# Kernel optimization log

Measured on AMD Instinct MI355X. Metric: run time of the kernel, lower is better.

The kernel has to match this reference:

```python
import jax, jax.numpy as jnp
import numpy as np

NUM_NODES = 50000
NUM_EDGES = 600000
HIDDEN = 128


def setup_inputs() -> dict:
    key = jax.random.key(0)
    ks = jax.random.split(key, 8)
    edge_index = jax.random.randint(ks[0], (2, NUM_EDGES), 0, NUM_NODES, dtype=jnp.int32)
    # xavier-uniform-ish init for node embeddings and GCN weights
    lim_emb = float(np.sqrt(6.0 / (NUM_NODES + HIDDEN)))
    node_emb = jax.random.uniform(ks[1], (NUM_NODES, HIDDEN), jnp.float32, -lim_emb, lim_emb)
    lim_w = float(np.sqrt(6.0 / (HIDDEN + HIDDEN)))
    W0 = jax.random.uniform(ks[2], (HIDDEN, HIDDEN), jnp.float32, -lim_w, lim_w)
    W1 = jax.random.uniform(ks[3], (HIDDEN, HIDDEN), jnp.float32, -lim_w, lim_w)
    W2 = jax.random.uniform(ks[4], (HIDDEN, HIDDEN), jnp.float32, -lim_w, lim_w)
    b0 = jnp.zeros((HIDDEN,), jnp.float32)
    b1 = jnp.zeros((HIDDEN,), jnp.float32)
    b2 = jnp.zeros((HIDDEN,), jnp.float32)
    return {"edge_index": edge_index, "node_emb": node_emb,
            "W0": W0, "b0": b0, "W1": W1, "b1": b1, "W2": W2, "b2": b2}


def _gcn_conv(x, W, b, src, dst, norm, n):
    # PyG GCNConv: linear transform, then sym-normalized scatter-sum + bias
    h = x @ W                                  # [N, H]
    msg = h[src] * norm[:, None]               # [E+N, H] gather + scale
    out = jax.ops.segment_sum(msg, dst, num_segments=n)  # scatter-sum
    return out + b


def reference(edge_index, node_emb, W0, b0, W1, b1, W2, b2):
    n = node_emb.shape[0]
    loop = jnp.arange(n, dtype=edge_index.dtype)
    src = jnp.concatenate([edge_index[0], loop])   # add self-loops
    dst = jnp.concatenate([edge_index[1], loop])
    deg = jnp.zeros((n,), node_emb.dtype).at[dst].add(1.0)
    dinv = jax.lax.rsqrt(deg)                      # deg >= 1 due to self-loops
    norm = dinv[src] * dinv[dst]                   # [E+N]

    x = node_emb
    x = _gcn_conv(x, W0, b0, src, dst, norm, n)
    x = jax.nn.relu(x)                             # dropout in eval mode: identity
    x = _gcn_conv(x, W1, b1, src, dst, norm, n)
    x = jax.nn.relu(x)
    x = _gcn_conv(x, W2, b2, src, dst, norm, n)
    return x
```

## Files before the change

### kernel.cpp

```cpp
#include <hip/hip_runtime.h>
#include <hip/hip_fp16.h>

#define N_NODES 50000
#define N_EDGES 600000
#define HID 128
#define CAP 64

typedef _Float16 half8 __attribute__((ext_vector_type(8)));
typedef float f32x4 __attribute__((ext_vector_type(4)));

union Pack8 {
    _Float16 h[8];
    uint4 u;
};


__global__ __launch_bounds__(256) void k_init(int* __restrict__ cnt,
                                              const float* __restrict__ W0,
                                              const float* __restrict__ W1,
                                              const float* __restrict__ W2,
                                              _Float16* __restrict__ Wt) {
    int i = blockIdx.x * 256 + threadIdx.x;
    if (i < N_NODES) cnt[i] = 0;
    if (i < 3 * HID * HID) {
        int l = i >> 14;
        int r = i & 16383;
        int n = r >> 7, k = r & 127;
        const float* W = (l == 0) ? W0 : (l == 1) ? W1 : W2;
        Wt[i] = (_Float16)W[k * HID + n];
    }
}


__global__ __launch_bounds__(256) void k_bucket(const int* __restrict__ src,
                                                const int* __restrict__ dst,
                                                int* __restrict__ cnt,
                                                int* __restrict__ bkt) {
    int e = blockIdx.x * 256 + threadIdx.x;
    if (e >= N_EDGES) return;
    int d = dst[e];
    int pos = atomicAdd(&cnt[d], 1);
    if (pos < CAP) bkt[d * CAP + pos] = src[e];
}


__global__ __launch_bounds__(512) void k_gemm0(const float* __restrict__ X,
                                               const _Float16* __restrict__ Wt,
                                               const int* __restrict__ cnt,
                                               _Float16* __restrict__ HS) {
    __shared__ _Float16 Xl[128][136];
    __shared__ _Float16 Wl[128][136];

    const int tid = threadIdx.x;
    const int row0 = blockIdx.x * 128;

#pragma unroll
    for (int j = 0; j < 8; ++j) {
        int idx = tid + j * 512;
        int r = idx >> 5, p = idx & 31;
        float4 v = make_float4(0.f, 0.f, 0.f, 0.f);
        if (row0 + r < N_NODES) v = ((const float4*)X)[(size_t)(row0 + r) * 32 + p];
        _Float16* d = &Xl[r][p * 4];
        d[0] = (_Float16)v.x; d[1] = (_Float16)v.y;
        d[2] = (_Float16)v.z; d[3] = (_Float16)v.w;
    }
#pragma unroll
    for (int j = 0; j < 4; ++j) {
        int idx = tid + j * 512;
        int r = idx >> 4, p = idx & 15;
        *(uint4*)&Wl[r][p * 8] = ((const uint4*)Wt)[idx];
    }
    __syncthreads();

    const int w = tid >> 6;
    const int l = tid & 63;
    const int m16 = l & 15;
    const int kg = l >> 4;

    f32x4 acc[8];
#pragma unroll
    for (int nt = 0; nt < 8; ++nt) acc[nt] = (f32x4)(0.f);
#pragma unroll
    for (int ks = 0; ks < 4; ++ks) {
        half8 a = *(const half8*)&Xl[w * 16 + m16][kg * 8 + ks * 32];
#pragma unroll
        for (int nt = 0; nt < 8; ++nt) {
            half8 b = *(const half8*)&Wl[nt * 16 + m16][kg * 8 + ks * 32];
            acc[nt] = __builtin_amdgcn_mfma_f32_16x16x32_f16(a, b, acc[nt], 0, 0, 0);
        }
    }

    const int rbase = row0 + w * 16 + kg * 4;
#pragma unroll
    for (int j = 0; j < 4; ++j) {
        int r = rbase + j;
        if (r < N_NODES) {
            float dv = rsqrtf((float)(cnt[r] + 1));
#pragma unroll
            for (int nt = 0; nt < 8; ++nt)
                HS[(size_t)r * HID + nt * 16 + m16] = (_Float16)(acc[nt][j] * dv);
        }
    }
}


__global__ __launch_bounds__(512) void k_fused(const _Float16* __restrict__ hsIn,
                                               const int* __restrict__ bkt,
                                               const int* __restrict__ cnt,
                                               const float* __restrict__ bias,
                                               const _Float16* __restrict__ Wt,
                                               _Float16* __restrict__ hsOut) {
    __shared__ _Float16 Xl[128][136];
    __shared__ _Float16 Wl[128][136];

    const int tid = threadIdx.x;
    const int row0 = blockIdx.x * 128;

#pragma unroll
    for (int j = 0; j < 4; ++j) {
        int idx = tid + j * 512;
        int r = idx >> 4, p = idx & 15;
        *(uint4*)&Wl[r][p * 8] = ((const uint4*)Wt)[idx];
    }

    const int grp = tid >> 4;
    const int c = (tid & 15) * 8;
    const _Float16* __restrict__ hc = hsIn + c;
    float4 bv0 = *(const float4*)&bias[c];
    float4 bv1 = *(const float4*)&bias[c + 4];
    float bb[8] = {bv0.x, bv0.y, bv0.z, bv0.w, bv1.x, bv1.y, bv1.z, bv1.w};

#pragma unroll
    for (int rnd = 0; rnd < 4; ++rnd) {
        int rl = rnd * 32 + grp;
        int node = row0 + rl;
        Pack8 pk;
        if (node < N_NODES) {
            float a[8], a2[8];
            {
                Pack8 v;
                v.u = *(const uint4*)&hc[(size_t)node * HID];
#pragma unroll
                for (int j = 0; j < 8; ++j) { a[j] = (float)v.h[j]; a2[j] = 0.f; }
            }
            const int* __restrict__ row = bkt + node * CAP;
            int ne = cnt[node];
            int e = 0;
            for (; e + 4 <= ne; e += 4) {
                int4 s4 = *(const int4*)&row[e];
                Pack8 v0, v1, v2, v3;
                v0.u = *(const uint4*)&hc[(size_t)s4.x * HID];
                v1.u = *(const uint4*)&hc[(size_t)s4.y * HID];
                v2.u = *(const uint4*)&hc[(size_t)s4.z * HID];
                v3.u = *(const uint4*)&hc[(size_t)s4.w * HID];
#pragma unroll
                for (int j = 0; j < 8; ++j) {
                    a[j] += (float)v0.h[j] + (float)v1.h[j];
                    a2[j] += (float)v2.h[j] + (float)v3.h[j];
                }
            }
            if (e + 2 <= ne) {
                int s0 = row[e], s1 = row[e + 1];
                Pack8 v0, v1;
                v0.u = *(const uint4*)&hc[(size_t)s0 * HID];
                v1.u = *(const uint4*)&hc[(size_t)s1 * HID];
#pragma unroll
                for (int j = 0; j < 8; ++j) a[j] += (float)v0.h[j] + (float)v1.h[j];
                e += 2;
            }
            if (e < ne) {
                int s0 = row[e];
                Pack8 v0;
                v0.u = *(const uint4*)&hc[(size_t)s0 * HID];
#pragma unroll
                for (int j = 0; j < 8; ++j) a[j] += (float)v0.h[j];
            }
            float dv = rsqrtf((float)(ne + 1));
#pragma unroll
            for (int j = 0; j < 8; ++j)
                pk.h[j] = (_Float16)fmaxf(bb[j] + dv * (a[j] + a2[j]), 0.f);
        } else {
            pk.u = make_uint4(0, 0, 0, 0);
        }
        *(uint4*)&Xl[rl][c] = pk.u;
    }
    __syncthreads();

    const int w = tid >> 6;
    const int l = tid & 63;
    const int m16 = l & 15;
    const int kg = l >> 4;

    f32x4 acc[8];
#pragma unroll
    for (int nt = 0; nt < 8; ++nt) acc[nt] = (f32x4)(0.f);
#pragma unroll
    for (int ks = 0; ks < 4; ++ks) {
        half8 a = *(const half8*)&Xl[w * 16 + m16][kg * 8 + ks * 32];
#pragma unroll
        for (int nt = 0; nt < 8; ++nt) {
            half8 b = *(const half8*)&Wl[nt * 16 + m16][kg * 8 + ks * 32];
            acc[nt] = __builtin_amdgcn_mfma_f32_16x16x32_f16(a, b, acc[nt], 0, 0, 0);
        }
    }

    const int rbase = row0 + w * 16 + kg * 4;
#pragma unroll
    for (int j = 0; j < 4; ++j) {
        int r = rbase + j;
        if (r < N_NODES) {
            float dv = rsqrtf((float)(cnt[r] + 1));
#pragma unroll
            for (int nt = 0; nt < 8; ++nt)
                hsOut[(size_t)r * HID + nt * 16 + m16] = (_Float16)(acc[nt][j] * dv);
        }
    }
}


__global__ __launch_bounds__(256) void k_gather_out(const _Float16* __restrict__ hs,
                                                    const int* __restrict__ bkt,
                                                    const int* __restrict__ cnt,
                                                    const float* __restrict__ bias,
                                                    float* __restrict__ out) {
    int t = blockIdx.x * 256 + threadIdx.x;
    int node = t >> 4;
    if (node >= N_NODES) return;
    int c = (t & 15) * 8;

    const _Float16* __restrict__ hc = hs + c;

    float a[8], a2[8];
    {
        Pack8 v;
        v.u = *(const uint4*)&hc[(size_t)node * HID];
#pragma unroll
        for (int j = 0; j < 8; ++j) { a[j] = (float)v.h[j]; a2[j] = 0.f; }
    }
    const int* __restrict__ row = bkt + node * CAP;
    int ne = cnt[node];
    int e = 0;
    for (; e + 4 <= ne; e += 4) {
        int4 s4 = *(const int4*)&row[e];
        Pack8 v0, v1, v2, v3;
        v0.u = *(const uint4*)&hc[(size_t)s4.x * HID];
        v1.u = *(const uint4*)&hc[(size_t)s4.y * HID];
        v2.u = *(const uint4*)&hc[(size_t)s4.z * HID];
        v3.u = *(const uint4*)&hc[(size_t)s4.w * HID];
#pragma unroll
        for (int j = 0; j < 8; ++j) {
            a[j] += (float)v0.h[j] + (float)v1.h[j];
            a2[j] += (float)v2.h[j] + (float)v3.h[j];
        }
    }
    if (e + 2 <= ne) {
        int s0 = row[e], s1 = row[e + 1];
        Pack8 v0, v1;
        v0.u = *(const uint4*)&hc[(size_t)s0 * HID];
        v1.u = *(const uint4*)&hc[(size_t)s1 * HID];
#pragma unroll
        for (int j = 0; j < 8; ++j) a[j] += (float)v0.h[j] + (float)v1.h[j];
        e += 2;
    }
    if (e < ne) {
        int s0 = row[e];
        Pack8 v0;
        v0.u = *(const uint4*)&hc[(size_t)s0 * HID];
#pragma unroll
        for (int j = 0; j < 8; ++j) a[j] += (float)v0.h[j];
    }

    float dv = rsqrtf((float)(ne + 1));
    float4 b0 = *(const float4*)&bias[c];
    float4 b1 = *(const float4*)&bias[c + 4];
    float bb[8] = {b0.x, b0.y, b0.z, b0.w, b1.x, b1.y, b1.z, b1.w};
    float4* op = (float4*)&out[(size_t)node * HID + c];
    op[0] = make_float4(bb[0] + dv * (a[0] + a2[0]), bb[1] + dv * (a[1] + a2[1]),
                        bb[2] + dv * (a[2] + a2[2]), bb[3] + dv * (a[3] + a2[3]));
    op[1] = make_float4(bb[4] + dv * (a[4] + a2[4]), bb[5] + dv * (a[5] + a2[5]),
                        bb[6] + dv * (a[6] + a2[6]), bb[7] + dv * (a[7] + a2[7]));
}


extern "C" void kernel_launch(void* const* d_in, const int* in_sizes, int n_in,
                              void* d_out, int out_size, void* d_ws, size_t ws_size,
                              hipStream_t stream) {
    const int* edge_index = (const int*)d_in[0];
    const float* node_emb = (const float*)d_in[1];
    const float* W0 = (const float*)d_in[2];
    const float* b0 = (const float*)d_in[3];
    const float* W1 = (const float*)d_in[4];
    const float* b1 = (const float*)d_in[5];
    const float* W2 = (const float*)d_in[6];
    const float* b2 = (const float*)d_in[7];
    float* out = (float*)d_out;

    const int* src = edge_index;
    const int* dst = edge_index + N_EDGES;

    float* ws = (float*)d_ws;
    int* cnt = (int*)ws;
    int* bkt = (int*)(ws + 50000);
    _Float16* hsA = (_Float16*)(ws + 3250000);
    _Float16* hsB = (_Float16*)(ws + 6450000);
    _Float16* Wt = (_Float16*)(ws + 9650000);

    const int tile_blocks = (N_NODES + 127) / 128;
    const int gath_blocks = (N_NODES * 16 + 255) / 256;
    const int edge_blocks = (N_EDGES + 255) / 256;
    const int init_blocks = (N_NODES + 255) / 256;

    k_init<<<init_blocks, 256, 0, stream>>>(cnt, W0, W1, W2, Wt);
    k_bucket<<<edge_blocks, 256, 0, stream>>>(src, dst, cnt, bkt);

    k_gemm0<<<tile_blocks, 512, 0, stream>>>(node_emb, Wt, cnt, hsA);
    k_fused<<<tile_blocks, 512, 0, stream>>>(hsA, bkt, cnt, b0, Wt + 16384, hsB);
    k_fused<<<tile_blocks, 512, 0, stream>>>(hsB, bkt, cnt, b1, Wt + 32768, hsA);
    k_gather_out<<<gath_blocks, 256, 0, stream>>>(hsA, bkt, cnt, b2, out);
}
```

Baseline: 158.7 us.

## Sort tile rows by degree to balance gather work across wavefronts

Adds a per-tile counting sort of the 128 nodes by in-degree in shared memory and uses the permutation to assign nodes to 16-lane groups in the fused aggregation and final gather kernels. Nodes with similar degree then share a wavefront, which cuts lane divergence in the variable-length neighbor loops. The final gather kernel is restructured to 512-thread tile blocks handling 4 rounds of nodes each. The cost is extra syncthreads and shared-memory atomics per block, plus fewer, larger blocks in the output kernel.

```diff
diff --git a/kernel.cpp b/kernel.cpp
--- a/kernel.cpp
+++ b/kernel.cpp
@@ -104,6 +104,35 @@
 }
 
 
+__device__ __forceinline__ void tile_sort(int tid, int row0,
+                                          const int* __restrict__ cnt,
+                                          unsigned char* tperm, short* lne,
+                                          int* lhist, int* lcur) {
+    if (tid < 64) { lhist[tid] = 0; lcur[tid] = 0; }
+    __syncthreads();
+    int myne = 0;
+    if (tid < 128) {
+        int node = row0 + tid;
+        myne = (node < N_NODES) ? cnt[node] : 0;
+        lne[tid] = (short)myne;
+        atomicAdd(&lhist[myne < 63 ? myne : 63], 1);
+    }
+    __syncthreads();
+    if (tid == 0) {
+        int s = 0;
+#pragma unroll
+        for (int b = 0; b < 64; ++b) { int x = lhist[b]; lhist[b] = s; s += x; }
+    }
+    __syncthreads();
+    if (tid < 128) {
+        int b = myne < 63 ? myne : 63;
+        int pos = lhist[b] + atomicAdd(&lcur[b], 1);
+        tperm[pos] = (unsigned char)tid;
+    }
+    __syncthreads();
+}
+
+
 __global__ __launch_bounds__(512) void k_fused(const _Float16* __restrict__ hsIn,
                                                const int* __restrict__ bkt,
                                                const int* __restrict__ cnt,
@@ -112,6 +141,9 @@
                                                _Float16* __restrict__ hsOut) {
     __shared__ _Float16 Xl[128][136];
     __shared__ _Float16 Wl[128][136];
+    __shared__ int lhist[64], lcur[64];
+    __shared__ unsigned char tperm[128];
+    __shared__ short lne[128];
 
     const int tid = threadIdx.x;
     const int row0 = blockIdx.x * 128;
@@ -122,6 +154,8 @@
         int r = idx >> 4, p = idx & 15;
         *(uint4*)&Wl[r][p * 8] = ((const uint4*)Wt)[idx];
     }
+
+    tile_sort(tid, row0, cnt, tperm, lne, lhist, lcur);
 
     const int grp = tid >> 4;
     const int c = (tid & 15) * 8;
@@ -132,7 +166,7 @@
 
 #pragma unroll
     for (int rnd = 0; rnd < 4; ++rnd) {
-        int rl = rnd * 32 + grp;
+        int rl = tperm[rnd * 32 + grp];
         int node = row0 + rl;
         Pack8 pk;
         if (node < N_NODES) {
@@ -144,7 +178,7 @@
                 for (int j = 0; j < 8; ++j) { a[j] = (float)v.h[j]; a2[j] = 0.f; }
             }
             const int* __restrict__ row = bkt + node * CAP;
-            int ne = cnt[node];
+            int ne = lne[rl];
             int e = 0;
             for (; e + 4 <= ne; e += 4) {
                 int4 s4 = *(const int4*)&row[e];
@@ -218,67 +252,79 @@
 }
 
 
-__global__ __launch_bounds__(256) void k_gather_out(const _Float16* __restrict__ hs,
+__global__ __launch_bounds__(512) void k_gather_out(const _Float16* __restrict__ hs,
                                                     const int* __restrict__ bkt,
                                                     const int* __restrict__ cnt,
                                                     const float* __restrict__ bias,
                                                     float* __restrict__ out) {
-    int t = blockIdx.x * 256 + threadIdx.x;
-    int node = t >> 4;
-    if (node >= N_NODES) return;
-    int c = (t & 15) * 8;
-
+    __shared__ int lhist[64], lcur[64];
+    __shared__ unsigned char tperm[128];
+    __shared__ short lne[128];
+
+    const int tid = threadIdx.x;
+    const int row0 = blockIdx.x * 128;
+
+    tile_sort(tid, row0, cnt, tperm, lne, lhist, lcur);
+
+    const int grp = tid >> 4;
+    const int c = (tid & 15) * 8;
     const _Float16* __restrict__ hc = hs + c;
-
-    float a[8], a2[8];
-    {
-        Pack8 v;
-        v.u = *(const uint4*)&hc[(size_t)node * HID];
-#pragma unroll
-        for (int j = 0; j < 8; ++j) { a[j] = (float)v.h[j]; a2[j] = 0.f; }
-    }
-    const int* __restrict__ row = bkt + node * CAP;
-    int ne = cnt[node];
-    int e = 0;
-    for (; e + 4 <= ne; e += 4) {
-        int4 s4 = *(const int4*)&row[e];
-        Pack8 v0, v1, v2, v3;
-        v0.u = *(const uint4*)&hc[(size_t)s4.x * HID];
-        v1.u = *(const uint4*)&hc[(size_t)s4.y * HID];
-        v2.u = *(const uint4*)&hc[(size_t)s4.z * HID];
-        v3.u = *(const uint4*)&hc[(size_t)s4.w * HID];
-#pragma unroll
-        for (int j = 0; j < 8; ++j) {
-            a[j] += (float)v0.h[j] + (float)v1.h[j];
-            a2[j] += (float)v2.h[j] + (float)v3.h[j];
-        }
-    }
-    if (e + 2 <= ne) {
-        int s0 = row[e], s1 = row[e + 1];
-        Pack8 v0, v1;
-        v0.u = *(const uint4*)&hc[(size_t)s0 * HID];
-        v1.u = *(const uint4*)&hc[(size_t)s1 * HID];
-#pragma unroll
-        for (int j = 0; j < 8; ++j) a[j] += (float)v0.h[j] + (float)v1.h[j];
-        e += 2;
-    }
-    if (e < ne) {
-        int s0 = row[e];
-        Pack8 v0;
-        v0.u = *(const uint4*)&hc[(size_t)s0 * HID];
-#pragma unroll
-        for (int j = 0; j < 8; ++j) a[j] += (float)v0.h[j];
-    }
-
-    float dv = rsqrtf((float)(ne + 1));
-    float4 b0 = *(const float4*)&bias[c];
-    float4 b1 = *(const float4*)&bias[c + 4];
-    float bb[8] = {b0.x, b0.y, b0.z, b0.w, b1.x, b1.y, b1.z, b1.w};
-    float4* op = (float4*)&out[(size_t)node * HID + c];
-    op[0] = make_float4(bb[0] + dv * (a[0] + a2[0]), bb[1] + dv * (a[1] + a2[1]),
-                        bb[2] + dv * (a[2] + a2[2]), bb[3] + dv * (a[3] + a2[3]));
-    op[1] = make_float4(bb[4] + dv * (a[4] + a2[4]), bb[5] + dv * (a[5] + a2[5]),
-                        bb[6] + dv * (a[6] + a2[6]), bb[7] + dv * (a[7] + a2[7]));
+    float4 bv0 = *(const float4*)&bias[c];
+    float4 bv1 = *(const float4*)&bias[c + 4];
+    float bb[8] = {bv0.x, bv0.y, bv0.z, bv0.w, bv1.x, bv1.y, bv1.z, bv1.w};
+
+#pragma unroll
+    for (int rnd = 0; rnd < 4; ++rnd) {
+        int rl = tperm[rnd * 32 + grp];
+        int node = row0 + rl;
+        if (node >= N_NODES) continue;
+        float a[8], a2[8];
+        {
+            Pack8 v;
+            v.u = *(const uint4*)&hc[(size_t)node * HID];
+#pragma unroll
+            for (int j = 0; j < 8; ++j) { a[j] = (float)v.h[j]; a2[j] = 0.f; }
+        }
+        const int* __restrict__ row = bkt + node * CAP;
+        int ne = lne[rl];
+        int e = 0;
+        for (; e + 4 <= ne; e += 4) {
+            int4 s4 = *(const int4*)&row[e];
+            Pack8 v0, v1, v2, v3;
+            v0.u = *(const uint4*)&hc[(size_t)s4.x * HID];
+            v1.u = *(const uint4*)&hc[(size_t)s4.y * HID];
+            v2.u = *(const uint4*)&hc[(size_t)s4.z * HID];
+            v3.u = *(const uint4*)&hc[(size_t)s4.w * HID];
+#pragma unroll
+            for (int j = 0; j < 8; ++j) {
+                a[j] += (float)v0.h[j] + (float)v1.h[j];
+                a2[j] += (float)v2.h[j] + (float)v3.h[j];
+            }
+        }
+        if (e + 2 <= ne) {
+            int s0 = row[e], s1 = row[e + 1];
+            Pack8 v0, v1;
+            v0.u = *(const uint4*)&hc[(size_t)s0 * HID];
+            v1.u = *(const uint4*)&hc[(size_t)s1 * HID];
+#pragma unroll
+            for (int j = 0; j < 8; ++j) a[j] += (float)v0.h[j] + (float)v1.h[j];
+            e += 2;
+        }
+        if (e < ne) {
+            int s0 = row[e];
+            Pack8 v0;
+            v0.u = *(const uint4*)&hc[(size_t)s0 * HID];
+#pragma unroll
+            for (int j = 0; j < 8; ++j) a[j] += (float)v0.h[j];
+        }
+
+        float dv = rsqrtf((float)(ne + 1));
+        float4* op = (float4*)&out[(size_t)node * HID + c];
+        op[0] = make_float4(bb[0] + dv * (a[0] + a2[0]), bb[1] + dv * (a[1] + a2[1]),
+                            bb[2] + dv * (a[2] + a2[2]), bb[3] + dv * (a[3] + a2[3]));
+        op[1] = make_float4(bb[4] + dv * (a[4] + a2[4]), bb[5] + dv * (a[5] + a2[5]),
+                            bb[6] + dv * (a[6] + a2[6]), bb[7] + dv * (a[7] + a2[7]));
+    }
 }
 
 
@@ -306,7 +352,6 @@
     _Float16* Wt = (_Float16*)(ws + 9650000);
 
     const int tile_blocks = (N_NODES + 127) / 128;
-    const int gath_blocks = (N_NODES * 16 + 255) / 256;
     const int edge_blocks = (N_EDGES + 255) / 256;
     const int init_blocks = (N_NODES + 255) / 256;
 
@@ -316,5 +361,5 @@
     k_gemm0<<<tile_blocks, 512, 0, stream>>>(node_emb, Wt, cnt, hsA);
     k_fused<<<tile_blocks, 512, 0, stream>>>(hsA, bkt, cnt, b0, Wt + 16384, hsB);
     k_fused<<<tile_blocks, 512, 0, stream>>>(hsB, bkt, cnt, b1, Wt + 32768, hsA);
-    k_gather_out<<<gath_blocks, 256, 0, stream>>>(hsA, bkt, cnt, b2, out);
-}
+    k_gather_out<<<tile_blocks, 512, 0, stream>>>(hsA, bkt, cnt, b2, out);
+}
```

Result: no change. 158.3 us, median of 2 (-0.2%).

## Halve fused tile to 64 rows and sort rows by degree for gather balance

Applied to the files above, without the earlier changes.

The fused gather+GEMM kernel now processes 64 nodes per block instead of 128, doubling the block count, and raises the occupancy hint via launch bounds. Within each block, nodes are counting-sorted by in-degree so that 16-lane groups handling rows in the same round have similar edge counts, reducing divergence and tail imbalance. The GEMM stage is re-split so each of the eight waves computes a 16x64 quarter tile. The cost is extra shared-memory histogram work and syncs, plus reloading W into LDS for twice as many blocks.

```diff
diff --git a/kernel.cpp b/kernel.cpp
--- a/kernel.cpp
+++ b/kernel.cpp
@@ -104,17 +104,20 @@
 }
 
 
-__global__ __launch_bounds__(512) void k_fused(const _Float16* __restrict__ hsIn,
-                                               const int* __restrict__ bkt,
-                                               const int* __restrict__ cnt,
-                                               const float* __restrict__ bias,
-                                               const _Float16* __restrict__ Wt,
-                                               _Float16* __restrict__ hsOut) {
-    __shared__ _Float16 Xl[128][136];
+__global__ __launch_bounds__(512, 6) void k_fused(const _Float16* __restrict__ hsIn,
+                                                  const int* __restrict__ bkt,
+                                                  const int* __restrict__ cnt,
+                                                  const float* __restrict__ bias,
+                                                  const _Float16* __restrict__ Wt,
+                                                  _Float16* __restrict__ hsOut) {
+    __shared__ _Float16 Xl[64][136];
     __shared__ _Float16 Wl[128][136];
+    __shared__ int lhist[64], lcur[64];
+    __shared__ unsigned char tperm[64];
+    __shared__ short lne[64];
 
     const int tid = threadIdx.x;
-    const int row0 = blockIdx.x * 128;
+    const int row0 = blockIdx.x * 64;
 
 #pragma unroll
     for (int j = 0; j < 4; ++j) {
@@ -122,6 +125,29 @@
         int r = idx >> 4, p = idx & 15;
         *(uint4*)&Wl[r][p * 8] = ((const uint4*)Wt)[idx];
     }
+
+    if (tid < 64) { lhist[tid] = 0; lcur[tid] = 0; }
+    __syncthreads();
+    int myne = 0;
+    if (tid < 64) {
+        int node = row0 + tid;
+        myne = (node < N_NODES) ? cnt[node] : 0;
+        lne[tid] = (short)myne;
+        atomicAdd(&lhist[myne < 63 ? myne : 63], 1);
+    }
+    __syncthreads();
+    if (tid == 0) {
+        int s = 0;
+#pragma unroll
+        for (int b = 0; b < 64; ++b) { int x = lhist[b]; lhist[b] = s; s += x; }
+    }
+    __syncthreads();
+    if (tid < 64) {
+        int b = myne < 63 ? myne : 63;
+        int pos = lhist[b] + atomicAdd(&lcur[b], 1);
+        tperm[pos] = (unsigned char)tid;
+    }
+    __syncthreads();
 
     const int grp = tid >> 4;
     const int c = (tid & 15) * 8;
@@ -131,8 +157,8 @@
     float bb[8] = {bv0.x, bv0.y, bv0.z, bv0.w, bv1.x, bv1.y, bv1.z, bv1.w};
 
 #pragma unroll
-    for (int rnd = 0; rnd < 4; ++rnd) {
-        int rl = rnd * 32 + grp;
+    for (int rnd = 0; rnd < 2; ++rnd) {
+        int rl = tperm[rnd * 32 + grp];
         int node = row0 + rl;
         Pack8 pk;
         if (node < N_NODES) {
@@ -144,7 +170,7 @@
                 for (int j = 0; j < 8; ++j) { a[j] = (float)v.h[j]; a2[j] = 0.f; }
             }
             const int* __restrict__ row = bkt + node * CAP;
-            int ne = cnt[node];
+            int ne = lne[rl];
             int e = 0;
             for (; e + 4 <= ne; e += 4) {
                 int4 s4 = *(const int4*)&row[e];
@@ -187,32 +213,34 @@
     __syncthreads();
 
     const int w = tid >> 6;
+    const int wr = w >> 1;
+    const int wc = w & 1;
     const int l = tid & 63;
     const int m16 = l & 15;
     const int kg = l >> 4;
 
-    f32x4 acc[8];
-#pragma unroll
-    for (int nt = 0; nt < 8; ++nt) acc[nt] = (f32x4)(0.f);
+    f32x4 acc[4];
+#pragma unroll
+    for (int nt = 0; nt < 4; ++nt) acc[nt] = (f32x4)(0.f);
 #pragma unroll
     for (int ks = 0; ks < 4; ++ks) {
-        half8 a = *(const half8*)&Xl[w * 16 + m16][kg * 8 + ks * 32];
-#pragma unroll
-        for (int nt = 0; nt < 8; ++nt) {
-            half8 b = *(const half8*)&Wl[nt * 16 + m16][kg * 8 + ks * 32];
+        half8 a = *(const half8*)&Xl[wr * 16 + m16][kg * 8 + ks * 32];
+#pragma unroll
+        for (int nt = 0; nt < 4; ++nt) {
+            half8 b = *(const half8*)&Wl[wc * 64 + nt * 16 + m16][kg * 8 + ks * 32];
             acc[nt] = __builtin_amdgcn_mfma_f32_16x16x32_f16(a, b, acc[nt], 0, 0, 0);
         }
     }
 
-    const int rbase = row0 + w * 16 + kg * 4;
+    const int rbase = row0 + wr * 16 + kg * 4;
 #pragma unroll
     for (int j = 0; j < 4; ++j) {
         int r = rbase + j;
         if (r < N_NODES) {
             float dv = rsqrtf((float)(cnt[r] + 1));
 #pragma unroll
-            for (int nt = 0; nt < 8; ++nt)
-                hsOut[(size_t)r * HID + nt * 16 + m16] = (_Float16)(acc[nt][j] * dv);
+            for (int nt = 0; nt < 4; ++nt)
+                hsOut[(size_t)r * HID + wc * 64 + nt * 16 + m16] = (_Float16)(acc[nt][j] * dv);
         }
     }
 }
@@ -305,7 +333,8 @@
     _Float16* hsB = (_Float16*)(ws + 6450000);
     _Float16* Wt = (_Float16*)(ws + 9650000);
 
-    const int tile_blocks = (N_NODES + 127) / 128;
+    const int gemm_blocks = (N_NODES + 127) / 128;
+    const int fuse_blocks = (N_NODES + 63) / 64;
     const int gath_blocks = (N_NODES * 16 + 255) / 256;
     const int edge_blocks = (N_EDGES + 255) / 256;
     const int init_blocks = (N_NODES + 255) / 256;
@@ -313,8 +342,8 @@
     k_init<<<init_blocks, 256, 0, stream>>>(cnt, W0, W1, W2, Wt);
     k_bucket<<<edge_blocks, 256, 0, stream>>>(src, dst, cnt, bkt);
 
-    k_gemm0<<<tile_blocks, 512, 0, stream>>>(node_emb, Wt, cnt, hsA);
-    k_fused<<<tile_blocks, 512, 0, stream>>>(hsA, bkt, cnt, b0, Wt + 16384, hsB);
-    k_fused<<<tile_blocks, 512, 0, stream>>>(hsB, bkt, cnt, b1, Wt + 32768, hsA);
+    k_gemm0<<<gemm_blocks, 512, 0, stream>>>(node_emb, Wt, cnt, hsA);
+    k_fused<<<fuse_blocks, 512, 0, stream>>>(hsA, bkt, cnt, b0, Wt + 16384, hsB);
+    k_fused<<<fuse_blocks, 512, 0, stream>>>(hsB, bkt, cnt, b1, Wt + 32768, hsA);
     k_gather_out<<<gath_blocks, 256, 0, stream>>>(hsA, bkt, cnt, b2, out);
 }
```

After: 172.8 us. +8.9%, slower.

## Slice features into column panels, compact CSR with 16-bit indices, unfuse gather from GEMM

Applied to the files above, without the earlier changes.

Stores intermediate features in eight 16-column slices so each gather block works on one 32-byte slice per node, aiming to keep the gathered working set of a slice in L2. Adds a compaction pass that builds CSR offsets and a 16-bit source-index array from the bucket lists, which shrinks index traffic. Within each block, nodes are sorted by degree to balance per-lane work. The previous fused gather+GEMM kernel is split into separate gather and GEMM launches, which adds launches and a round trip of the aggregated features through memory. The 16-bit indices cannot represent node ids of 65536 or more, so the code is tied to this node count.

```diff
diff --git a/kernel.cpp b/kernel.cpp
--- a/kernel.cpp
+++ b/kernel.cpp
@@ -5,6 +5,7 @@
 #define N_EDGES 600000
 #define HID 128
 #define CAP 64
+#define SLICE 800000
 
 typedef _Float16 half8 __attribute__((ext_vector_type(8)));
 typedef float f32x4 __attribute__((ext_vector_type(4)));
@@ -16,12 +17,14 @@
 
 
 __global__ __launch_bounds__(256) void k_init(int* __restrict__ cnt,
+                                              int* __restrict__ gcur,
                                               const float* __restrict__ W0,
                                               const float* __restrict__ W1,
                                               const float* __restrict__ W2,
                                               _Float16* __restrict__ Wt) {
     int i = blockIdx.x * 256 + threadIdx.x;
     if (i < N_NODES) cnt[i] = 0;
+    if (i == 0) *gcur = 0;
     if (i < 3 * HID * HID) {
         int l = i >> 14;
         int r = i & 16383;
@@ -44,6 +47,37 @@
 }
 
 
+__global__ __launch_bounds__(256) void k_compact(const int* __restrict__ cnt,
+                                                 const int* __restrict__ bkt,
+                                                 int* __restrict__ gcur,
+                                                 int* __restrict__ offs,
+                                                 unsigned short* __restrict__ csr16) {
+    __shared__ int buf[256];
+    __shared__ int sbase;
+    const int t = threadIdx.x;
+    const int n = blockIdx.x * 256 + t;
+    int ne = (n < N_NODES) ? cnt[n] : 0;
+    buf[t] = ne;
+    __syncthreads();
+#pragma unroll
+    for (int off = 1; off < 256; off <<= 1) {
+        int x = (t >= off) ? buf[t - off] : 0;
+        __syncthreads();
+        buf[t] += x;
+        __syncthreads();
+    }
+    int incl = buf[t];
+    if (t == 255) sbase = atomicAdd(gcur, buf[255]);
+    __syncthreads();
+    if (n < N_NODES) {
+        int off = sbase + incl - ne;
+        offs[n] = off;
+        const int* row = bkt + n * CAP;
+        for (int j = 0; j < ne; ++j) csr16[off + j] = (unsigned short)row[j];
+    }
+}
+
+
 __global__ __launch_bounds__(512) void k_gemm0(const float* __restrict__ X,
                                                const _Float16* __restrict__ Wt,
                                                const int* __restrict__ cnt,
@@ -98,91 +132,39 @@
             float dv = rsqrtf((float)(cnt[r] + 1));
 #pragma unroll
             for (int nt = 0; nt < 8; ++nt)
-                HS[(size_t)r * HID + nt * 16 + m16] = (_Float16)(acc[nt][j] * dv);
-        }
-    }
-}
-
-
-__global__ __launch_bounds__(512) void k_fused(const _Float16* __restrict__ hsIn,
-                                               const int* __restrict__ bkt,
+                HS[(size_t)nt * SLICE + (size_t)r * 16 + m16] = (_Float16)(acc[nt][j] * dv);
+        }
+    }
+}
+
+
+__global__ __launch_bounds__(512) void k_gemmS(const _Float16* __restrict__ xh,
+                                               const _Float16* __restrict__ Wt,
                                                const int* __restrict__ cnt,
-                                               const float* __restrict__ bias,
-                                               const _Float16* __restrict__ Wt,
-                                               _Float16* __restrict__ hsOut) {
+                                               _Float16* __restrict__ HS) {
     __shared__ _Float16 Xl[128][136];
     __shared__ _Float16 Wl[128][136];
 
     const int tid = threadIdx.x;
     const int row0 = blockIdx.x * 128;
 
+#pragma unroll
+    for (int j = 0; j < 4; ++j) {
+        int idx = tid + j * 512;
+        int s = idx >> 8;
+        int u = idx & 255;
+        int r = u >> 1, half = u & 1;
+        uint4 v = make_uint4(0, 0, 0, 0);
+        int node = row0 + r;
+        if (node < N_NODES)
+            v = *(const uint4*)&xh[(size_t)s * SLICE + (size_t)node * 16 + half * 8];
+        *(uint4*)&Xl[r][s * 16 + half * 8] = v;
+    }
 #pragma unroll
     for (int j = 0; j < 4; ++j) {
         int idx = tid + j * 512;
         int r = idx >> 4, p = idx & 15;
         *(uint4*)&Wl[r][p * 8] = ((const uint4*)Wt)[idx];
-    }
-
-    const int grp = tid >> 4;
-    const int c = (tid & 15) * 8;
-    const _Float16* __restrict__ hc = hsIn + c;
-    float4 bv0 = *(const float4*)&bias[c];
-    float4 bv1 = *(const float4*)&bias[c + 4];
-    float bb[8] = {bv0.x, bv0.y, bv0.z, bv0.w, bv1.x, bv1.y, bv1.z, bv1.w};
-
-#pragma unroll
-    for (int rnd = 0; rnd < 4; ++rnd) {
-        int rl = rnd * 32 + grp;
-        int node = row0 + rl;
-        Pack8 pk;
-        if (node < N_NODES) {
-            float a[8], a2[8];
-            {
-                Pack8 v;
-                v.u = *(const uint4*)&hc[(size_t)node * HID];
-#pragma unroll
-                for (int j = 0; j < 8; ++j) { a[j] = (float)v.h[j]; a2[j] = 0.f; }
-            }
-            const int* __restrict__ row = bkt + node * CAP;
-            int ne = cnt[node];
-            int e = 0;
-            for (; e + 4 <= ne; e += 4) {
-                int4 s4 = *(const int4*)&row[e];
-                Pack8 v0, v1, v2, v3;
-                v0.u = *(const uint4*)&hc[(size_t)s4.x * HID];
-                v1.u = *(const uint4*)&hc[(size_t)s4.y * HID];
-                v2.u = *(const uint4*)&hc[(size_t)s4.z * HID];
-                v3.u = *(const uint4*)&hc[(size_t)s4.w * HID];
-#pragma unroll
-                for (int j = 0; j < 8; ++j) {
-                    a[j] += (float)v0.h[j] + (float)v1.h[j];
-                    a2[j] += (float)v2.h[j] + (float)v3.h[j];
-                }
-            }
-            if (e + 2 <= ne) {
-                int s0 = row[e], s1 = row[e + 1];
-                Pack8 v0, v1;
-                v0.u = *(const uint4*)&hc[(size_t)s0 * HID];
-                v1.u = *(const uint4*)&hc[(size_t)s1 * HID];
-#pragma unroll
-                for (int j = 0; j < 8; ++j) a[j] += (float)v0.h[j] + (float)v1.h[j];
-                e += 2;
-            }
-            if (e < ne) {
-                int s0 = row[e];
-                Pack8 v0;
-                v0.u = *(const uint4*)&hc[(size_t)s0 * HID];
-#pragma unroll
-                for (int j = 0; j < 8; ++j) a[j] += (float)v0.h[j];
-            }
-            float dv = rsqrtf((float)(ne + 1));
-#pragma unroll
-            for (int j = 0; j < 8; ++j)
-                pk.h[j] = (_Float16)fmaxf(bb[j] + dv * (a[j] + a2[j]), 0.f);
-        } else {
-            pk.u = make_uint4(0, 0, 0, 0);
-        }
-        *(uint4*)&Xl[rl][c] = pk.u;
     }
     __syncthreads();
 
@@ -212,73 +194,108 @@
             float dv = rsqrtf((float)(cnt[r] + 1));
 #pragma unroll
             for (int nt = 0; nt < 8; ++nt)
-                hsOut[(size_t)r * HID + nt * 16 + m16] = (_Float16)(acc[nt][j] * dv);
-        }
-    }
-}
-
-
-__global__ __launch_bounds__(256) void k_gather_out(const _Float16* __restrict__ hs,
-                                                    const int* __restrict__ bkt,
-                                                    const int* __restrict__ cnt,
-                                                    const float* __restrict__ bias,
-                                                    float* __restrict__ out) {
-    int t = blockIdx.x * 256 + threadIdx.x;
-    int node = t >> 4;
+                HS[(size_t)nt * SLICE + (size_t)r * 16 + m16] = (_Float16)(acc[nt][j] * dv);
+        }
+    }
+}
+
+
+template <int MODE>
+__global__ __launch_bounds__(256) void k_gatherS(const _Float16* __restrict__ hsS,
+                                                 const unsigned short* __restrict__ csr16,
+                                                 const int* __restrict__ offs,
+                                                 const int* __restrict__ cnt,
+                                                 const float* __restrict__ bias,
+                                                 _Float16* __restrict__ xh,
+                                                 float* __restrict__ out) {
+    __shared__ int lhist[64], lcur[64];
+    __shared__ unsigned char tperm[128];
+    __shared__ short lne[128];
+
+    const int tid = threadIdx.x;
+    const int slice = blockIdx.x & 7;
+    const int row0 = (blockIdx.x >> 3) * 128;
+
+    if (tid < 64) { lhist[tid] = 0; lcur[tid] = 0; }
+    __syncthreads();
+    int myne = 0;
+    if (tid < 128) {
+        int node = row0 + tid;
+        myne = (node < N_NODES) ? cnt[node] : 0;
+        lne[tid] = (short)myne;
+        atomicAdd(&lhist[myne < 63 ? myne : 63], 1);
+    }
+    __syncthreads();
+    if (tid == 0) {
+        int s = 0;
+#pragma unroll
+        for (int b = 0; b < 64; ++b) { int x = lhist[b]; lhist[b] = s; s += x; }
+    }
+    __syncthreads();
+    if (tid < 128) {
+        int b = myne < 63 ? myne : 63;
+        int pos = lhist[b] + atomicAdd(&lcur[b], 1);
+        tperm[pos] = (unsigned char)tid;
+    }
+    __syncthreads();
+
+    const int p = tid >> 1;
+    const int half = tid & 1;
+    const int rl = tperm[p];
+    const int node = row0 + rl;
     if (node >= N_NODES) return;
-    int c = (t & 15) * 8;
-
-    const _Float16* __restrict__ hc = hs + c;
+
+    const _Float16* __restrict__ hsl = hsS + (size_t)slice * SLICE + half * 8;
 
     float a[8], a2[8];
     {
         Pack8 v;
-        v.u = *(const uint4*)&hc[(size_t)node * HID];
+        v.u = *(const uint4*)&hsl[(size_t)node * 16];
 #pragma unroll
         for (int j = 0; j < 8; ++j) { a[j] = (float)v.h[j]; a2[j] = 0.f; }
     }
-    const int* __restrict__ row = bkt + node * CAP;
-    int ne = cnt[node];
+    int ne = lne[rl];
+    int base = offs[node];
     int e = 0;
-    for (; e + 4 <= ne; e += 4) {
-        int4 s4 = *(const int4*)&row[e];
-        Pack8 v0, v1, v2, v3;
-        v0.u = *(const uint4*)&hc[(size_t)s4.x * HID];
-        v1.u = *(const uint4*)&hc[(size_t)s4.y * HID];
-        v2.u = *(const uint4*)&hc[(size_t)s4.z * HID];
-        v3.u = *(const uint4*)&hc[(size_t)s4.w * HID];
+    for (; e + 2 <= ne; e += 2) {
+        int s0 = csr16[base + e], s1 = csr16[base + e + 1];
+        Pack8 v0, v1;
+        v0.u = *(const uint4*)&hsl[(size_t)s0 * 16];
+        v1.u = *(const uint4*)&hsl[(size_t)s1 * 16];
 #pragma unroll
         for (int j = 0; j < 8; ++j) {
-            a[j] += (float)v0.h[j] + (float)v1.h[j];
-            a2[j] += (float)v2.h[j] + (float)v3.h[j];
-        }
-    }
-    if (e + 2 <= ne) {
-        int s0 = row[e], s1 = row[e + 1];
-        Pack8 v0, v1;
-        v0.u = *(const uint4*)&hc[(size_t)s0 * HID];
-        v1.u = *(const uint4*)&hc[(size_t)s1 * HID];
-#pragma unroll
-        for (int j = 0; j < 8; ++j) a[j] += (float)v0.h[j] + (float)v1.h[j];
-        e += 2;
+            a[j] += (float)v0.h[j];
+            a2[j] += (float)v1.h[j];
+        }
     }
     if (e < ne) {
-        int s0 = row[e];
+        int s0 = csr16[base + e];
         Pack8 v0;
-        v0.u = *(const uint4*)&hc[(size_t)s0 * HID];
+        v0.u = *(const uint4*)&hsl[(size_t)s0 * 16];
 #pragma unroll
         for (int j = 0; j < 8; ++j) a[j] += (float)v0.h[j];
     }
 
     float dv = rsqrtf((float)(ne + 1));
+    const int c = slice * 16 + half * 8;
     float4 b0 = *(const float4*)&bias[c];
     float4 b1 = *(const float4*)&bias[c + 4];
     float bb[8] = {b0.x, b0.y, b0.z, b0.w, b1.x, b1.y, b1.z, b1.w};
-    float4* op = (float4*)&out[(size_t)node * HID + c];
-    op[0] = make_float4(bb[0] + dv * (a[0] + a2[0]), bb[1] + dv * (a[1] + a2[1]),
-                        bb[2] + dv * (a[2] + a2[2]), bb[3] + dv * (a[3] + a2[3]));
-    op[1] = make_float4(bb[4] + dv * (a[4] + a2[4]), bb[5] + dv * (a[5] + a2[5]),
-                        bb[6] + dv * (a[6] + a2[6]), bb[7] + dv * (a[7] + a2[7]));
+
+    if constexpr (MODE == 0) {
+        Pack8 pk;
+#pragma unroll
+        for (int j = 0; j < 8; ++j)
+            pk.h[j] = (_Float16)fmaxf(bb[j] + dv * (a[j] + a2[j]), 0.f);
+        *(uint4*)&xh[(size_t)slice * SLICE + (size_t)node * 16 + half * 8] = pk.u;
+    } else {
+        float o[8];
+#pragma unroll
+        for (int j = 0; j < 8; ++j) o[j] = bb[j] + dv * (a[j] + a2[j]);
+        float4* op = (float4*)&out[(size_t)node * HID + c];
+        op[0] = make_float4(o[0], o[1], o[2], o[3]);
+        op[1] = make_float4(o[4], o[5], o[6], o[7]);
+    }
 }
 
 
@@ -300,21 +317,28 @@
 
     float* ws = (float*)d_ws;
     int* cnt = (int*)ws;
-    int* bkt = (int*)(ws + 50000);
-    _Float16* hsA = (_Float16*)(ws + 3250000);
-    _Float16* hsB = (_Float16*)(ws + 6450000);
-    _Float16* Wt = (_Float16*)(ws + 9650000);
+    int* offs = (int*)(ws + 50000);
+    int* gcur = (int*)(ws + 100000);
+    unsigned short* csr16 = (unsigned short*)(ws + 100004);
+    int* bkt = (int*)(ws + 400008);
+    _Float16* xh = (_Float16*)(ws + 400008);
+    _Float16* hsA = (_Float16*)(ws + 3600008);
+    _Float16* hsB = (_Float16*)(ws + 6800008);
+    _Float16* Wt = (_Float16*)(ws + 10000008);
 
     const int tile_blocks = (N_NODES + 127) / 128;
-    const int gath_blocks = (N_NODES * 16 + 255) / 256;
+    const int gath_blocks = tile_blocks * 8;
     const int edge_blocks = (N_EDGES + 255) / 256;
     const int init_blocks = (N_NODES + 255) / 256;
 
-    k_init<<<init_blocks, 256, 0, stream>>>(cnt, W0, W1, W2, Wt);
+    k_init<<<init_blocks, 256, 0, stream>>>(cnt, gcur, W0, W1, W2, Wt);
     k_bucket<<<edge_blocks, 256, 0, stream>>>(src, dst, cnt, bkt);
+    k_compact<<<init_blocks, 256, 0, stream>>>(cnt, bkt, gcur, offs, csr16);
 
     k_gemm0<<<tile_blocks, 512, 0, stream>>>(node_emb, Wt, cnt, hsA);
-    k_fused<<<tile_blocks, 512, 0, stream>>>(hsA, bkt, cnt, b0, Wt + 16384, hsB);
-    k_fused<<<tile_blocks, 512, 0, stream>>>(hsB, bkt, cnt, b1, Wt + 32768, hsA);
-    k_gather_out<<<gath_blocks, 256, 0, stream>>>(hsA, bkt, cnt, b2, out);
-}
+    k_gatherS<0><<<gath_blocks, 256, 0, stream>>>(hsA, csr16, offs, cnt, b0, xh, nullptr);
+    k_gemmS<<<tile_blocks, 512, 0, stream>>>(xh, Wt + 16384, cnt, hsB);
+    k_gatherS<0><<<gath_blocks, 256, 0, stream>>>(hsB, csr16, offs, cnt, b1, xh, nullptr);
+    k_gemmS<<<tile_blocks, 512, 0, stream>>>(xh, Wt + 32768, cnt, hsA);
+    k_gatherS<1><<<gath_blocks, 256, 0, stream>>>(hsA, csr16, offs, cnt, b2, nullptr, out);
+}
```

New measurement: 175.6 us. +10.7%, slower.
